# Kernel optimization log

Hardware: AMD Instinct MI355X
Metric: run time of the kernel (lower is better)

## Reference

```python
import jax, jax.numpy as jnp
import numpy as np

D_STATE = 32

def _layernorm(x, g, b, eps=1e-5):
    m = jnp.mean(x, -1, keepdims=True)
    v = jnp.mean((x - m) ** 2, -1, keepdims=True)
    return (x - m) * jax.lax.rsqrt(v + eps) * g + b

def _mlp(x, W1, b1, W2, b2):
    return jax.nn.relu(x @ W1 + b1) @ W2 + b2

def _mamba_block(x, Win, Wconv, bconv, Wxproj, Wdt, bdt, Alog, Dp, Wout):
    Bsz, T, _ = x.shape
    d_inner = Wconv.shape[0]
    dt_rank = Wdt.shape[0]
    xz = x @ Win                                   # [B,T,2*d_inner]
    xi, res = jnp.split(xz, 2, axis=-1)
    K = Wconv.shape[1]
    xp = jnp.pad(xi, ((0, 0), (K - 1, 0), (0, 0)))  # causal depthwise conv
    xi = sum(xp[:, k:k + T, :] * Wconv[:, k] for k in range(K)) + bconv
    xi = jax.nn.silu(xi)
    xdbl = xi @ Wxproj                              # [B,T,dt_rank+2*ds]
    dtr = xdbl[..., :dt_rank]
    Bm = xdbl[..., dt_rank:dt_rank + D_STATE]
    Cm = xdbl[..., dt_rank + D_STATE:]
    dt = jax.nn.softplus(dtr @ Wdt + bdt)           # [B,T,d_inner]
    A = -jnp.exp(Alog)                              # [d_inner, ds]

    def step(h, inp):
        dt_t, B_t, C_t, x_t = inp                   # [B,di],[B,ds],[B,ds],[B,di]
        dA = jnp.exp(dt_t[:, :, None] * A)          # [B,di,ds]
        dBx = (dt_t * x_t)[:, :, None] * B_t[:, None, :]
        h = dA * h + dBx
        return h, jnp.einsum('bds,bs->bd', h, C_t)

    h0 = jnp.zeros((Bsz, d_inner, D_STATE), xi.dtype)
    _, ys = jax.lax.scan(step, h0, (jnp.swapaxes(dt, 0, 1), jnp.swapaxes(Bm, 0, 1),
                                    jnp.swapaxes(Cm, 0, 1), jnp.swapaxes(xi, 0, 1)))
    y = jnp.swapaxes(ys, 0, 1) + xi * Dp
    y = y * jax.nn.silu(res)
    return y @ Wout

def _dynamics(z, Win, Wconv, bconv, Wxproj, Wdt, bdt, Alog, Dp, Wout, gamma, beta):
    out = z
    for i in range(Win.shape[0]):  # 2 stacked residual Mamba blocks
        out = out + _mamba_block(out, Win[i], Wconv[i], bconv[i], Wxproj[i],
                                 Wdt[i], bdt[i], Alog[i], Dp[i], Wout[i])
    return _layernorm(out, gamma, beta)

def setup_inputs():
    key = jax.random.key(0)
    Bz, T, IN, D, DI, DTR, K, NB = 8, 1024, 32, 64, 128, 4, 4, 2
    ks = iter(jax.random.split(key, 32))
    n = lambda shape, s=0.02: jax.random.normal(next(ks), shape, jnp.float32) * s
    return {
        'x': jax.random.normal(next(ks), (Bz, T, IN), jnp.float32),
        'We1': n((IN, 64)), 'be1': jnp.zeros((64,)),
        'We2': n((64, D)), 'be2': jnp.zeros((D,)),
        'Wd1': n((D, 64)), 'bd1': jnp.zeros((64,)),
        'Wd2': n((64, IN)), 'bd2': jnp.zeros((IN,)),
        'Win': n((NB, D, 2 * DI)),
        'Wconv': n((NB, DI, K), 0.1), 'bconv': jnp.zeros((NB, DI)),
        'Wxproj': n((NB, DI, DTR + 2 * D_STATE)),
        'Wdt': n((NB, DTR, DI), 0.1), 'bdt': jnp.full((NB, DI), -4.0),
        'Alog': jnp.tile(jnp.log(jnp.arange(1.0, 33.0)), (NB, DI, 1)),
        'Dparam': jnp.ones((NB, DI)),
        'Wout': n((NB, DI, D)),
        'gamma': jnp.ones((D,)), 'beta': jnp.zeros((D,)),
        'pred_len': 4,
    }

def reference(x, We1, be1, We2, be2, Wd1, bd1, Wd2, bd2, Win, Wconv, bconv,
              Wxproj, Wdt, bdt, Alog, Dparam, Wout, gamma, beta, pred_len):
    z = _mlp(x, We1, be1, We2, be2)
    x_rec = _mlp(z, Wd1, bd1, Wd2, bd2)
    dyn = lambda u: _dynamics(u, Win, Wconv, bconv, Wxproj, Wdt, bdt,
                              Alog, Dparam, Wout, gamma, beta)
    z_dyn = dyn(z)
    x_dyn = _mlp(z_dyn, Wd1, bd1, Wd2, bd2)
    x_pred = None
    if pred_len > 0:
        T = z.shape[1]
        curr = z
        preds = []
        for _ in range(pred_len):
            z_next = dyn(curr[:, -T:, :])[:, -1:, :]
            preds.append(z_next)
            curr = jnp.concatenate([curr, z_next], axis=1)
        x_pred = _mlp(jnp.concatenate(preds, axis=1), Wd1, bd1, Wd2, bd2)
    return (x_rec, x_dyn, x_pred, z, z_dyn)
```

## Files before the change

### kernel.cpp

```cpp
#include <hip/hip_runtime.h>

#define BSZ 8
#define TLEN 1024
#define DM 64
#define DI 128
#define DS 32
#define NCHUNK 16
#define CLEN 64
#define GEXT 1028

__device__ __forceinline__ float siluf(float x) { return x / (1.f + expf(-x)); }
__device__ __forceinline__ float softplusf(float x) { return (x > 20.f) ? x : log1pf(expf(x)); }

__global__ __launch_bounds__(256) void enc_xrec_kernel(
    const float* __restrict__ x,
    const float* __restrict__ We1, const float* __restrict__ be1,
    const float* __restrict__ We2, const float* __restrict__ be2,
    const float* __restrict__ Wd1, const float* __restrict__ bd1,
    const float* __restrict__ Wd2, const float* __restrict__ bd2,
    float* __restrict__ z, float* __restrict__ x_rec)
{
  __shared__ float s_x[16*32];
  __shared__ float s_h1[16*64];
  __shared__ float s_z[16*64];
  __shared__ float s_h2[16*64];
  const int tid = threadIdx.x;
  const int t0 = blockIdx.x * 16;
  s_x[tid]       = x[(size_t)t0*32 + tid];
  s_x[tid + 256] = x[(size_t)t0*32 + tid + 256];
  __syncthreads();
  const int j = tid & 63, tg = tid >> 6;
  {
    float w[32];
    #pragma unroll
    for (int k = 0; k < 32; k++) w[k] = We1[k*64 + j];
    #pragma unroll
    for (int q = 0; q < 4; q++) {
      int t = tg*4 + q;
      float a = be1[j];
      #pragma unroll
      for (int k = 0; k < 32; k++) a = fmaf(s_x[t*32 + k], w[k], a);
      s_h1[t*64 + j] = fmaxf(a, 0.f);
    }
  }
  __syncthreads();
  {
    float w[64];
    #pragma unroll
    for (int k = 0; k < 64; k++) w[k] = We2[k*64 + j];
    #pragma unroll
    for (int q = 0; q < 4; q++) {
      int t = tg*4 + q;
      float a = be2[j];
      #pragma unroll
      for (int k = 0; k < 64; k++) a = fmaf(s_h1[t*64 + k], w[k], a);
      s_z[t*64 + j] = a;
      z[(size_t)(t0 + t)*64 + j] = a;
    }
  }
  __syncthreads();
  {
    float w[64];
    #pragma unroll
    for (int k = 0; k < 64; k++) w[k] = Wd1[k*64 + j];
    #pragma unroll
    for (int q = 0; q < 4; q++) {
      int t = tg*4 + q;
      float a = bd1[j];
      #pragma unroll
      for (int k = 0; k < 64; k++) a = fmaf(s_z[t*64 + k], w[k], a);
      s_h2[t*64 + j] = fmaxf(a, 0.f);
    }
  }
  __syncthreads();
  {
    const int c = tid & 31, tg2 = tid >> 5;
    float w[64];
    #pragma unroll
    for (int k = 0; k < 64; k++) w[k] = Wd2[k*32 + c];
    #pragma unroll
    for (int q = 0; q < 2; q++) {
      int t = tg2*2 + q;
      float a = bd2[c];
      #pragma unroll
      for (int k = 0; k < 64; k++) a = fmaf(s_h2[t*64 + k], w[k], a);
      x_rec[(size_t)(t0 + t)*32 + c] = a;
    }
  }
}

__global__ __launch_bounds__(256,4) void pre_kernel(
    const float* __restrict__ in, int in_stride,
    const float* __restrict__ Win, const float* __restrict__ Wconv, const float* __restrict__ bconv,
    const float* __restrict__ Wxproj, const float* __restrict__ Wdt, const float* __restrict__ bdt,
    float* __restrict__ xibuf, float* __restrict__ resgbuf,
    float2* __restrict__ ddbuf, float* __restrict__ Bbuf, float* __restrict__ Cbuf,
    float* __restrict__ xzout)
{
  __shared__ float s_xi[8*128];
  __shared__ float s_dtr[8*4];
  const int tid = threadIdx.x;
  const int b  = blockIdx.x >> 7;
  const int t0 = (blockIdx.x & 127) * 8;

  const float* rowp[11];
  #pragma unroll
  for (int r = 0; r < 11; r++) {
    int tg = t0 - 3 + r;
    rowp[r] = (tg >= 0) ? in + ((size_t)b*in_stride + tg)*DM : in;
  }

  float acc[11];
  #pragma unroll
  for (int r = 0; r < 11; r++) acc[r] = 0.f;

  if (t0 > 0) {
    #pragma unroll
    for (int k4 = 0; k4 < 16; k4++) {
      float w0 = Win[(k4*4+0)*256 + tid];
      float w1 = Win[(k4*4+1)*256 + tid];
      float w2 = Win[(k4*4+2)*256 + tid];
      float w3 = Win[(k4*4+3)*256 + tid];
      #pragma unroll
      for (int r = 0; r < 11; r++) {
        float4 xv = *(const float4*)(rowp[r] + k4*4);
        acc[r] = fmaf(xv.x, w0, acc[r]);
        acc[r] = fmaf(xv.y, w1, acc[r]);
        acc[r] = fmaf(xv.z, w2, acc[r]);
        acc[r] = fmaf(xv.w, w3, acc[r]);
      }
    }
  } else {
    #pragma unroll
    for (int k4 = 0; k4 < 16; k4++) {
      float w0 = Win[(k4*4+0)*256 + tid];
      float w1 = Win[(k4*4+1)*256 + tid];
      float w2 = Win[(k4*4+2)*256 + tid];
      float w3 = Win[(k4*4+3)*256 + tid];
      #pragma unroll
      for (int r = 3; r < 11; r++) {
        float4 xv = *(const float4*)(rowp[r] + k4*4);
        acc[r] = fmaf(xv.x, w0, acc[r]);
        acc[r] = fmaf(xv.y, w1, acc[r]);
        acc[r] = fmaf(xv.z, w2, acc[r]);
        acc[r] = fmaf(xv.w, w3, acc[r]);
      }
    }
  }

  if (tid < 128) {
    float4 wc = *(const float4*)&Wconv[tid*4];
    float bc = bconv[tid];
    const bool store_xz = (t0 == TLEN-8);
    #pragma unroll
    for (int tau = 0; tau < 8; tau++) {
      float v = bc;
      v = fmaf(acc[tau+0], wc.x, v);
      v = fmaf(acc[tau+1], wc.y, v);
      v = fmaf(acc[tau+2], wc.z, v);
      v = fmaf(acc[tau+3], wc.w, v);
      float xiv = siluf(v);
      s_xi[tau*128 + tid] = xiv;
      xibuf[((size_t)b*TLEN + t0 + tau)*DI + tid] = xiv;
      if (store_xz) xzout[((size_t)b*GEXT + t0 + tau)*128 + tid] = acc[tau+3];
    }
  } else {
    int d = tid - 128;
    #pragma unroll
    for (int tau = 0; tau < 8; tau++)
      resgbuf[((size_t)b*TLEN + t0 + tau)*DI + d] = siluf(acc[tau+3]);
  }
  __syncthreads();
  {
    const int wv = tid >> 6, c = tid & 63;
    float a0 = 0.f, a1 = 0.f;
    const float4* x0 = (const float4*)&s_xi[(wv*2+0)*128];
    const float4* x1 = (const float4*)&s_xi[(wv*2+1)*128];
    #pragma unroll 4
    for (int k4 = 0; k4 < 32; k4++) {
      float wq0 = Wxproj[(k4*4+0)*68 + 4 + c];
      float wq1 = Wxproj[(k4*4+1)*68 + 4 + c];
      float wq2 = Wxproj[(k4*4+2)*68 + 4 + c];
      float wq3 = Wxproj[(k4*4+3)*68 + 4 + c];
      float4 v0 = x0[k4], v1 = x1[k4];
      a0 = fmaf(v0.x,wq0, fmaf(v0.y,wq1, fmaf(v0.z,wq2, fmaf(v0.w,wq3, a0))));
      a1 = fmaf(v1.x,wq0, fmaf(v1.y,wq1, fmaf(v1.z,wq2, fmaf(v1.w,wq3, a1))));
    }
    size_t tb = (size_t)b*TLEN + t0 + wv*2;
    if (c < 32) {
      Bbuf[(tb+0)*DS + c] = a0; Bbuf[(tb+1)*DS + c] = a1;
    } else {
      int cc = c - 32;
      Cbuf[(tb+0)*DS + cc] = a0; Cbuf[(tb+1)*DS + cc] = a1;
    }
  }
  if (tid < 32) {
    int tau = tid >> 2, cc = tid & 3;
    float a = 0.f;
    const float4* xx = (const float4*)&s_xi[tau*128];
    #pragma unroll 4
    for (int k4 = 0; k4 < 32; k4++) {
      float4 v = xx[k4];
      a = fmaf(v.x, Wxproj[(k4*4+0)*68 + cc], a);
      a = fmaf(v.y, Wxproj[(k4*4+1)*68 + cc], a);
      a = fmaf(v.z, Wxproj[(k4*4+2)*68 + cc], a);
      a = fmaf(v.w, Wxproj[(k4*4+3)*68 + cc], a);
    }
    s_dtr[tau*4 + cc] = a;
  }
  __syncthreads();
  #pragma unroll
  for (int u = 0; u < 4; u++) {
    int i = tid + u*256;
    int tau = i >> 7, d = i & 127;
    float a = bdt[d];
    #pragma unroll
    for (int r = 0; r < 4; r++) a = fmaf(s_dtr[tau*4 + r], Wdt[r*128 + d], a);
    float dtv = softplusf(a);
    ddbuf[((size_t)b*TLEN + t0 + tau)*DI + d] = make_float2(dtv, dtv * s_xi[i]);
  }
}

#define BSWZ(row3) (((row3)&3)<<1)

__device__ __forceinline__ int xcd_wid_4096() {
  return (blockIdx.x >> 3) | ((blockIdx.x & 7) << 9);
}

__global__ __launch_bounds__(128) void scan1_kernel(
    const float2* __restrict__ ddbuf, const float* __restrict__ Bbuf,
    const float* __restrict__ Alog, float2* __restrict__ hc)
{
  __shared__ float2 s_dd[4][CLEN];
  __shared__ float  s_Bt[32][68];
  const int tid = threadIdx.x;
  const int ch = tid >> 5, s = tid & 31;
  const int wid = xcd_wid_4096();
  const int dg = wid & 31;
  const int c  = (wid >> 5) & 15;
  const int b  = wid >> 9;
  const int d0 = dg * 4;
  const float A = -__expf(Alog[(d0 + ch)*DS + s]);
  const float2* ddg = ddbuf + ((size_t)b*TLEN + c*CLEN)*DI + d0;
  const float*  Bg  = Bbuf  + ((size_t)b*TLEN + c*CLEN)*DS;
  {
    int t = tid >> 1, half = tid & 1;
    float4 rdd = *(const float4*)((const float*)(ddg + (size_t)t*DI) + half*4);
    s_dd[2*half+0][t] = make_float2(rdd.x, rdd.y);
    s_dd[2*half+1][t] = make_float2(rdd.z, rdd.w);
    #pragma unroll
    for (int j = 0; j < 4; j++) {
      int q = tid + 128*j; int tt = q >> 3, k4 = q & 7;
      float4 rB = *(const float4*)(Bg + tt*DS + k4*4);
      int cp = (((tt>>2) ^ BSWZ(k4>>1)) << 2) + (tt & 3);
      s_Bt[k4*4+0][cp] = rB.x; s_Bt[k4*4+1][cp] = rB.y;
      s_Bt[k4*4+2][cp] = rB.z; s_Bt[k4*4+3][cp] = rB.w;
    }
  }
  __syncthreads();
  float h = 0.f, dts = 0.f;
  const float4* dd4 = (const float4*)&s_dd[ch][0];
  const float4* bt4 = (const float4*)&s_Bt[s][0];
  const int swr = BSWZ(s>>3);
  #pragma unroll
  for (int j = 0; j < 8; j++) {
    float4 e0 = dd4[4*j+0], e1 = dd4[4*j+1], e2 = dd4[4*j+2], e3 = dd4[4*j+3];
    float4 bb0 = bt4[(2*j)^swr], bb1 = bt4[(2*j+1)^swr];
    h = fmaf(__expf(e0.x*A), h, e0.y*bb0.x);
    h = fmaf(__expf(e0.z*A), h, e0.w*bb0.y);
    h = fmaf(__expf(e1.x*A), h, e1.y*bb0.z);
    h = fmaf(__expf(e1.z*A), h, e1.w*bb0.w);
    h = fmaf(__expf(e2.x*A), h, e2.y*bb1.x);
    h = fmaf(__expf(e2.z*A), h, e2.w*bb1.y);
    h = fmaf(__expf(e3.x*A), h, e3.y*bb1.z);
    h = fmaf(__expf(e3.z*A), h, e3.w*bb1.w);
    dts += (e0.x + e0.z) + (e1.x + e1.z) + (e2.x + e2.z) + (e3.x + e3.z);
  }
  int o = ((b*NCHUNK + c)*DI + d0 + ch)*DS + s;
  hc[o] = make_float2(h, __expf(A*dts));
}

__global__ __launch_bounds__(128) void scan3_kernel(
    const float2* __restrict__ ddbuf, const float* __restrict__ Bbuf, const float* __restrict__ Cbuf,
    const float* __restrict__ Alog, const float2* __restrict__ hc, float* __restrict__ ysbuf,
    float* __restrict__ hout)
{
  __shared__ float2 s_dd[4][CLEN];
  __shared__ float  s_Bt[32][68];
  __shared__ float  s_Ct[32][68];
  __shared__ float  s_p[128][33];
  const int tid = threadIdx.x;
  const int ch = tid >> 5, s = tid & 31;
  const int wid = xcd_wid_4096();
  const int dg = wid & 31;
  const int c  = (wid >> 5) & 15;
  const int b  = wid >> 9;
  const int d0 = dg * 4;
  const float A = -__expf(Alog[(d0 + ch)*DS + s]);
  const float2* ddg = ddbuf + ((size_t)b*TLEN + c*CLEN)*DI + d0;
  const float*  Bg  = Bbuf  + ((size_t)b*TLEN + c*CLEN)*DS;
  const float*  Cg  = Cbuf  + ((size_t)b*TLEN + c*CLEN)*DS;

  const int ob = (d0 + ch)*DS + s;
  float2 v[15];
  #pragma unroll
  for (int q = 0; q < 15; q++) v[q] = hc[(size_t)(b*NCHUNK + q)*4096 + ob];

  {
    int t = tid >> 1, half = tid & 1;
    float4 rdd = *(const float4*)((const float*)(ddg + (size_t)t*DI) + half*4);
    s_dd[2*half+0][t] = make_float2(rdd.x, rdd.y);
    s_dd[2*half+1][t] = make_float2(rdd.z, rdd.w);
    #pragma unroll
    for (int j = 0; j < 4; j++) {
      int q = tid + 128*j; int tt = q >> 3, k4 = q & 7;
      float4 rB = *(const float4*)(Bg + tt*DS + k4*4);
      float4 rC = *(const float4*)(Cg + tt*DS + k4*4);
      int cp = (((tt>>2) ^ BSWZ(k4>>1)) << 2) + (tt & 3);
      s_Bt[k4*4+0][cp] = rB.x; s_Bt[k4*4+1][cp] = rB.y;
      s_Bt[k4*4+2][cp] = rB.z; s_Bt[k4*4+3][cp] = rB.w;
      s_Ct[k4*4+0][cp] = rC.x; s_Ct[k4*4+1][cp] = rC.y;
      s_Ct[k4*4+2][cp] = rC.z; s_Ct[k4*4+3][cp] = rC.w;
    }
  }
  float h = 0.f;
  #pragma unroll
  for (int q = 0; q < 15; q++)
    if (q < c) h = fmaf(v[q].y, h, v[q].x);
  __syncthreads();

  const float4* dd4 = (const float4*)&s_dd[ch][0];
  const float4* bt4 = (const float4*)&s_Bt[s][0];
  const float4* ct4 = (const float4*)&s_Ct[s][0];
  const int swr = BSWZ(s>>3);
  float* pr = &s_p[tid][0];
  #pragma unroll
  for (int half = 0; half < 2; half++) {
    #pragma unroll
    for (int j = 0; j < 4; j++) {
      const int jj = half*4 + j;
      float4 e0 = dd4[4*jj+0], e1 = dd4[4*jj+1], e2 = dd4[4*jj+2], e3 = dd4[4*jj+3];
      float4 bb0 = bt4[(2*jj)^swr], bb1 = bt4[(2*jj+1)^swr];
      float4 cc0 = ct4[(2*jj)^swr], cc1 = ct4[(2*jj+1)^swr];
      h = fmaf(__expf(e0.x*A), h, e0.y*bb0.x); pr[8*j+0] = h*cc0.x;
      h = fmaf(__expf(e0.z*A), h, e0.w*bb0.y); pr[8*j+1] = h*cc0.y;
      h = fmaf(__expf(e1.x*A), h, e1.y*bb0.z); pr[8*j+2] = h*cc0.z;
      h = fmaf(__expf(e1.z*A), h, e1.w*bb0.w); pr[8*j+3] = h*cc0.w;
      h = fmaf(__expf(e2.x*A), h, e2.y*bb1.x); pr[8*j+4] = h*cc1.x;
      h = fmaf(__expf(e2.z*A), h, e2.w*bb1.y); pr[8*j+5] = h*cc1.y;
      h = fmaf(__expf(e3.x*A), h, e3.y*bb1.z); pr[8*j+6] = h*cc1.z;
      h = fmaf(__expf(e3.z*A), h, e3.w*bb1.w); pr[8*j+7] = h*cc1.w;
    }
    __syncthreads();
    {
      const int ch2 = tid & 3;
      const int tq  = tid >> 2;
      float a = 0.f;
      #pragma unroll
      for (int s2 = 0; s2 < 32; s2++) a += s_p[ch2*32 + s2][tq];
      ysbuf[(size_t)(b*TLEN + c*CLEN + half*32 + tq)*DI + d0 + ch2] = a;
    }
    __syncthreads();
  }
  if (c == 15) hout[(size_t)(b*DI + d0 + ch)*DS + s] = h;
}

__global__ __launch_bounds__(256,4) void post_kernel(
    const float* __restrict__ ysbuf, const float* __restrict__ xibuf, const float* __restrict__ resgbuf,
    const float* __restrict__ Dp, const float* __restrict__ Wout,
    const float* __restrict__ basebuf, int base_stride,
    float* __restrict__ curg, float* __restrict__ zdyn, float* __restrict__ predz,
    const float* __restrict__ gamma, const float* __restrict__ beta,
    const float* __restrict__ Wd1, const float* __restrict__ bd1,
    const float* __restrict__ Wd2, const float* __restrict__ bd2,
    float* __restrict__ xdyn, int mode)
{
  __shared__ float s_y[8*128];
  __shared__ float s_z[8*64];
  __shared__ float s_h[8*64];
  const int tid = threadIdx.x;
  const int b  = blockIdx.x >> 7;
  const int t0 = (blockIdx.x & 127) * 8;
  #pragma unroll
  for (int u = 0; u < 4; u++) {
    int i = tid + u*256;
    size_t g = (size_t)(b*TLEN + t0)*DI + i;
    s_y[i] = (ysbuf[g] + xibuf[g]*Dp[i & 127]) * resgbuf[g];
  }
  __syncthreads();
  #pragma unroll
  for (int u = 0; u < 2; u++) {
    int i = tid + u*256;
    int tau = i >> 6, c = i & 63;
    float a = 0.f;
    const float4* yy = (const float4*)&s_y[tau*128];
    #pragma unroll 4
    for (int k4 = 0; k4 < 32; k4++) {
      float4 vv = yy[k4];
      a = fmaf(vv.x, Wout[(k4*4+0)*64 + c], a);
      a = fmaf(vv.y, Wout[(k4*4+1)*64 + c], a);
      a = fmaf(vv.z, Wout[(k4*4+2)*64 + c], a);
      a = fmaf(vv.w, Wout[(k4*4+3)*64 + c], a);
    }
    float base = basebuf[((size_t)b*base_stride + t0 + tau)*DM + c];
    float val = base + a;
    if (mode == 0) {
      curg[((size_t)b*GEXT + t0 + tau)*DM + c] = val;
    } else {
      float sum = val;
      #pragma unroll
      for (int m = 1; m < 64; m <<= 1) sum += __shfl_xor(sum, m);
      float mean = sum * (1.f/64.f);
      float dv = val - mean;
      float vs = dv*dv;
      #pragma unroll
      for (int m = 1; m < 64; m <<= 1) vs += __shfl_xor(vs, m);
      float oln = dv * rsqrtf(vs*(1.f/64.f) + 1e-5f) * gamma[c] + beta[c];
      zdyn[(size_t)(b*TLEN + t0 + tau)*DM + c] = oln;
      s_z[tau*64 + c] = oln;
      if (t0 + tau == TLEN-1) predz[(size_t)(b*4 + 0)*DM + c] = oln;
    }
  }
  if (mode == 1) {
    __syncthreads();
    #pragma unroll
    for (int u = 0; u < 2; u++) {
      int i = tid + u*256;
      int t = i >> 6, j = i & 63;
      float a = bd1[j];
      const float4* zz = (const float4*)&s_z[t*64];
      #pragma unroll 4
      for (int k4 = 0; k4 < 16; k4++) {
        float4 zv = zz[k4];
        a = fmaf(zv.x, Wd1[(k4*4+0)*64 + j], a);
        a = fmaf(zv.y, Wd1[(k4*4+1)*64 + j], a);
        a = fmaf(zv.z, Wd1[(k4*4+2)*64 + j], a);
        a = fmaf(zv.w, Wd1[(k4*4+3)*64 + j], a);
      }
      s_h[i] = fmaxf(a, 0.f);
    }
    __syncthreads();
    {
      int t = tid >> 5, c = tid & 31;
      float a = bd2[c];
      const float4* hh = (const float4*)&s_h[t*64];
      #pragma unroll 4
      for (int k4 = 0; k4 < 16; k4++) {
        float4 hv = hh[k4];
        a = fmaf(hv.x, Wd2[(k4*4+0)*32 + c], a);
        a = fmaf(hv.y, Wd2[(k4*4+1)*32 + c], a);
        a = fmaf(hv.z, Wd2[(k4*4+2)*32 + c], a);
        a = fmaf(hv.w, Wd2[(k4*4+3)*32 + c], a);
      }
      xdyn[(size_t)(b*TLEN + t0 + t)*32 + c] = a;
    }
  }
}

__device__ __forceinline__ void mamba_token(
    int tid, int b, int gn, const float* __restrict__ s_in,
    float* __restrict__ xzg, float* __restrict__ hbuf,
    const float* __restrict__ Win, const float* __restrict__ Wcv, const float* __restrict__ bcv,
    const float* __restrict__ Wxp, const float* __restrict__ Wdt, const float* __restrict__ bdt,
    const float* __restrict__ Al, const float* __restrict__ Dpp, const float* __restrict__ Wo,
    float* __restrict__ s_xz, float* __restrict__ s_xi, float* __restrict__ s_rg,
    float* __restrict__ s_dt, float* __restrict__ s_B, float* __restrict__ s_C,
    float* __restrict__ s_dtr, float* __restrict__ s_yp, float* __restrict__ s_y,
    float* __restrict__ s_ssm)
{
  {
    float a = 0.f;
    #pragma unroll
    for (int k = 0; k < 64; k++) a = fmaf(s_in[k], Win[k*256 + tid], a);
    s_xz[tid] = a;
  }
  __syncthreads();
  if (tid < 128) {
    xzg[((size_t)b*GEXT + gn)*128 + tid] = s_xz[tid];
    float acc = bcv[tid];
    acc = fmaf(xzg[((size_t)b*GEXT + gn-3)*128 + tid], Wcv[tid*4+0], acc);
    acc = fmaf(xzg[((size_t)b*GEXT + gn-2)*128 + tid], Wcv[tid*4+1], acc);
    acc = fmaf(xzg[((size_t)b*GEXT + gn-1)*128 + tid], Wcv[tid*4+2], acc);
    acc = fmaf(s_xz[tid], Wcv[tid*4+3], acc);
    s_xi[tid] = siluf(acc);
    s_rg[tid] = siluf(s_xz[128 + tid]);
  }
  __syncthreads();
  if (tid < 68) {
    float a = 0.f;
    #pragma unroll 4
    for (int k = 0; k < 128; k++) a = fmaf(s_xi[k], Wxp[k*68 + tid], a);
    if (tid < 4)       s_dtr[tid] = a;
    else if (tid < 36) s_B[tid-4] = a;
    else               s_C[tid-36] = a;
  }
  __syncthreads();
  if (tid < 128) {
    float a = bdt[tid];
    #pragma unroll
    for (int r = 0; r < 4; r++) a = fmaf(s_dtr[r], Wdt[r*128 + tid], a);
    s_dt[tid] = softplusf(a);
  }
  __syncthreads();
  {
    int d = tid >> 1, sh = (tid & 1) * 16;
    float dtd = s_dt[d], dtxd = dtd * s_xi[d];
    float yp = 0.f;
    #pragma unroll
    for (int q = 0; q < 16; q++) {
      int s = sh + q;
      size_t oo = (size_t)(b*DI + d)*DS + s;
      float A = -__expf(Al[d*DS + s]);
      float h = hbuf[oo];
      h = fmaf(__expf(dtd*A), h, dtxd*s_B[s]);
      hbuf[oo] = h;
      yp = fmaf(s_C[s], h, yp);
    }
    s_yp[(tid & 1)*128 + d] = yp;
  }
  __syncthreads();
  if (tid < 128) s_y[tid] = ((s_yp[tid] + s_yp[128 + tid]) + s_xi[tid]*Dpp[tid]) * s_rg[tid];
  __syncthreads();
  if (tid < 64) {
    float a = 0.f;
    #pragma unroll 4
    for (int k = 0; k < 128; k++) a = fmaf(s_y[k], Wo[k*64 + tid], a);
    s_ssm[tid] = a;
  }
  __syncthreads();
}

__global__ __launch_bounds__(256) void ext_all_kernel(
    float* __restrict__ predz,
    float* __restrict__ xz0, float* __restrict__ xz1,
    float* __restrict__ hbuf0, float* __restrict__ hbuf1,
    const float* __restrict__ Win0, const float* __restrict__ Wcv0, const float* __restrict__ bcv0,
    const float* __restrict__ Wxp0, const float* __restrict__ Wdt0, const float* __restrict__ bdt0,
    const float* __restrict__ Al0, const float* __restrict__ Dp0, const float* __restrict__ Wo0,
    const float* __restrict__ Win1, const float* __restrict__ Wcv1, const float* __restrict__ bcv1,
    const float* __restrict__ Wxp1, const float* __restrict__ Wdt1, const float* __restrict__ bdt1,
    const float* __restrict__ Al1, const float* __restrict__ Dp1, const float* __restrict__ Wo1,
    const float* __restrict__ gamma, const float* __restrict__ beta,
    const float* __restrict__ Wd1, const float* __restrict__ bd1,
    const float* __restrict__ Wd2, const float* __restrict__ bd2,
    float* __restrict__ x_pred)
{
  __shared__ float s_in[64], s_cg[64], s_ssm[64];
  __shared__ float s_xz[256], s_yp[256];
  __shared__ float s_xi[128], s_rg[128], s_dt[128], s_y[128];
  __shared__ float s_B[32], s_C[32], s_dtr[4];
  __shared__ float s_pz[4][64];
  __shared__ float s_h[4][64];
  const int tid = threadIdx.x;
  const int b = blockIdx.x;

  if (tid < 64) s_pz[0][tid] = predz[(size_t)(b*4 + 0)*DM + tid];
  __syncthreads();

  for (int p = 1; p <= 3; p++) {
    const int gn = 1023 + p;
    if (tid < 64) s_in[tid] = s_pz[p-1][tid];
    __syncthreads();
    mamba_token(tid, b, gn, s_in, xz0, hbuf0, Win0, Wcv0, bcv0, Wxp0, Wdt0, bdt0,
                Al0, Dp0, Wo0, s_xz, s_xi, s_rg, s_dt, s_B, s_C, s_dtr, s_yp, s_y, s_ssm);
    if (tid < 64) {
      float cg = s_in[tid] + s_ssm[tid];
      s_cg[tid] = cg;
      s_in[tid] = cg;
    }
    __syncthreads();
    mamba_token(tid, b, gn, s_in, xz1, hbuf1, Win1, Wcv1, bcv1, Wxp1, Wdt1, bdt1,
                Al1, Dp1, Wo1, s_xz, s_xi, s_rg, s_dt, s_B, s_C, s_dtr, s_yp, s_y, s_ssm);
    if (tid < 64) {
      float val = s_cg[tid] + s_ssm[tid];
      float sum = val;
      #pragma unroll
      for (int m = 1; m < 64; m <<= 1) sum += __shfl_xor(sum, m);
      float mean = sum * (1.f/64.f);
      float dv = val - mean;
      float vs = dv*dv;
      #pragma unroll
      for (int m = 1; m < 64; m <<= 1) vs += __shfl_xor(vs, m);
      float oln = dv * rsqrtf(vs*(1.f/64.f) + 1e-5f) * gamma[tid] + beta[tid];
      predz[(size_t)(b*4 + p)*DM + tid] = oln;
      s_pz[p][tid] = oln;
    }
    __syncthreads();
  }

  {
    int t = tid >> 6, j = tid & 63;
    float a = bd1[j];
    const float4* zz = (const float4*)&s_pz[t][0];
    #pragma unroll 4
    for (int k4 = 0; k4 < 16; k4++) {
      float4 zv = zz[k4];
      a = fmaf(zv.x, Wd1[(k4*4+0)*64 + j], a);
      a = fmaf(zv.y, Wd1[(k4*4+1)*64 + j], a);
      a = fmaf(zv.z, Wd1[(k4*4+2)*64 + j], a);
      a = fmaf(zv.w, Wd1[(k4*4+3)*64 + j], a);
    }
    s_h[t][j] = fmaxf(a, 0.f);
  }
  __syncthreads();
  if (tid < 128) {
    int t = tid >> 5, c = tid & 31;
    float a = bd2[c];
    const float4* hh = (const float4*)&s_h[t][0];
    #pragma unroll 4
    for (int k4 = 0; k4 < 16; k4++) {
      float4 hv = hh[k4];
      a = fmaf(hv.x, Wd2[(k4*4+0)*32 + c], a);
      a = fmaf(hv.y, Wd2[(k4*4+1)*32 + c], a);
      a = fmaf(hv.z, Wd2[(k4*4+2)*32 + c], a);
      a = fmaf(hv.w, Wd2[(k4*4+3)*32 + c], a);
    }
    x_pred[(size_t)(b*4 + t)*32 + c] = a;
  }
}

extern "C" void kernel_launch(void* const* d_in, const int* in_sizes, int n_in,
                              void* d_out, int out_size, void* d_ws, size_t ws_size,
                              hipStream_t stream)
{
  (void)in_sizes; (void)n_in; (void)out_size; (void)ws_size;
  const float* x     = (const float*)d_in[0];
  const float* We1   = (const float*)d_in[1];
  const float* be1   = (const float*)d_in[2];
  const float* We2   = (const float*)d_in[3];
  const float* be2   = (const float*)d_in[4];
  const float* Wd1   = (const float*)d_in[5];
  const float* bd1   = (const float*)d_in[6];
  const float* Wd2   = (const float*)d_in[7];
  const float* bd2   = (const float*)d_in[8];
  const float* Win   = (const float*)d_in[9];
  const float* Wconv = (const float*)d_in[10];
  const float* bconv = (const float*)d_in[11];
  const float* Wxp   = (const float*)d_in[12];
  const float* Wdt   = (const float*)d_in[13];
  const float* bdt   = (const float*)d_in[14];
  const float* Alog  = (const float*)d_in[15];
  const float* Dp    = (const float*)d_in[16];
  const float* Wout  = (const float*)d_in[17];
  const float* gamma = (const float*)d_in[18];
  const float* beta  = (const float*)d_in[19];

  float* o      = (float*)d_out;
  float* x_rec  = o;
  float* x_dyn  = o + 262144;
  float* x_pred = o + 524288;
  float* z      = o + 525312;
  float* zdyn   = o + 1049600;

  float* w      = (float*)d_ws;
  float* xi0    = w;
  float* resg0  = xi0   + 1048576;
  float2* dd0   = (float2*)(resg0 + 1048576);
  float* Bb0    = resg0 + 1048576 + 2097152;
  float* Cb0    = Bb0   + 262144;
  float* xi1    = Cb0   + 262144;
  float* resg1  = xi1   + 1048576;
  float2* dd1   = (float2*)(resg1 + 1048576);
  float* Bb1    = resg1 + 1048576 + 2097152;
  float* Cb1    = Bb1   + 262144;
  float* ys     = Cb1   + 262144;
  float2* hc    = (float2*)(ys + 1048576);
  float* predz  = ys + 1048576 + 1048576;
  float* xz0    = predz + 2048;
  float* xz1    = xz0   + 1052672;
  float* curg   = xz1   + 1052672;
  float* hbuf0  = curg  + 526336;
  float* hbuf1  = hbuf0 + 32768;

  const float* Win0 = Win,   *Win1 = Win + 64*256;
  const float* Wcv0 = Wconv, *Wcv1 = Wconv + 128*4;
  const float* bcv0 = bconv, *bcv1 = bconv + 128;
  const float* Wxp0 = Wxp,   *Wxp1 = Wxp + 128*68;
  const float* Wdt0 = Wdt,   *Wdt1 = Wdt + 4*128;
  const float* bdt0 = bdt,   *bdt1 = bdt + 128;
  const float* Al0  = Alog,  *Al1  = Alog + 128*32;
  const float* Dp0  = Dp,    *Dp1  = Dp + 128;
  const float* Wo0  = Wout,  *Wo1  = Wout + 128*64;

  enc_xrec_kernel<<<dim3(512), dim3(256), 0, stream>>>(x, We1, be1, We2, be2, Wd1, bd1, Wd2, bd2, z, x_rec);

  pre_kernel<<<dim3(1024), dim3(256), 0, stream>>>(z, TLEN,
                                                   Win0, Wcv0, bcv0, Wxp0, Wdt0, bdt0,
                                                   xi0, resg0, dd0, Bb0, Cb0, xz0);
  scan1_kernel<<<dim3(4096), dim3(128), 0, stream>>>(dd0, Bb0, Al0, hc);
  scan3_kernel<<<dim3(4096), dim3(128), 0, stream>>>(dd0, Bb0, Cb0, Al0, hc, ys, hbuf0);
  post_kernel<<<dim3(1024), dim3(256), 0, stream>>>(ys, xi0, resg0, Dp0, Wo0,
                                                    z, TLEN, curg,
                                                    (float*)nullptr, (float*)nullptr,
                                                    (const float*)nullptr, (const float*)nullptr,
                                                    (const float*)nullptr, (const float*)nullptr,
                                                    (const float*)nullptr, (const float*)nullptr,
                                                    (float*)nullptr, 0);

  pre_kernel<<<dim3(1024), dim3(256), 0, stream>>>(curg, GEXT,
                                                   Win1, Wcv1, bcv1, Wxp1, Wdt1, bdt1,
                                                   xi1, resg1, dd1, Bb1, Cb1, xz1);
  scan1_kernel<<<dim3(4096), dim3(128), 0, stream>>>(dd1, Bb1, Al1, hc);
  scan3_kernel<<<dim3(4096), dim3(128), 0, stream>>>(dd1, Bb1, Cb1, Al1, hc, ys, hbuf1);
  post_kernel<<<dim3(1024), dim3(256), 0, stream>>>(ys, xi1, resg1, Dp1, Wo1,
                                                    curg, GEXT, (float*)nullptr,
                                                    zdyn, predz, gamma, beta,
                                                    Wd1, bd1, Wd2, bd2, x_dyn, 1);

  ext_all_kernel<<<dim3(8), dim3(256), 0, stream>>>(predz, xz0, xz1, hbuf0, hbuf1,
      Win0, Wcv0, bcv0, Wxp0, Wdt0, bdt0, Al0, Dp0, Wo0,
      Win1, Wcv1, bcv1, Wxp1, Wdt1, bdt1, Al1, Dp1, Wo1,
      gamma, beta, Wd1, bd1, Wd2, bd2, x_pred);
}
```

Measured before the change: 235.1 us.

## Fuse encoder MLP into block-0 pre kernel and block-0 post into block-1 pre

Merges the encoder/reconstruction MLP kernel with the first Mamba pre-processing kernel, and the first block's output projection/residual with the second block's pre-processing. Each fused block recomputes the 3 halo rows needed by the causal conv in shared memory instead of re-reading z/curg from global memory. This removes two kernel launches and the global round trips of z and curg as inputs, at the cost of redundant halo computation (11 rows for 8 tokens) and more shared memory per block.

After: 228.6 us. -2.7%, faster.

```diff
diff --git a/kernel.cpp b/kernel.cpp
--- a/kernel.cpp
+++ b/kernel.cpp
@@ -12,139 +12,31 @@
 __device__ __forceinline__ float siluf(float x) { return x / (1.f + expf(-x)); }
 __device__ __forceinline__ float softplusf(float x) { return (x > 20.f) ? x : log1pf(expf(x)); }
 
-__global__ __launch_bounds__(256) void enc_xrec_kernel(
-    const float* __restrict__ x,
-    const float* __restrict__ We1, const float* __restrict__ be1,
-    const float* __restrict__ We2, const float* __restrict__ be2,
-    const float* __restrict__ Wd1, const float* __restrict__ bd1,
-    const float* __restrict__ Wd2, const float* __restrict__ bd2,
-    float* __restrict__ z, float* __restrict__ x_rec)
-{
-  __shared__ float s_x[16*32];
-  __shared__ float s_h1[16*64];
-  __shared__ float s_z[16*64];
-  __shared__ float s_h2[16*64];
-  const int tid = threadIdx.x;
-  const int t0 = blockIdx.x * 16;
-  s_x[tid]       = x[(size_t)t0*32 + tid];
-  s_x[tid + 256] = x[(size_t)t0*32 + tid + 256];
-  __syncthreads();
-  const int j = tid & 63, tg = tid >> 6;
-  {
-    float w[32];
-    #pragma unroll
-    for (int k = 0; k < 32; k++) w[k] = We1[k*64 + j];
-    #pragma unroll
-    for (int q = 0; q < 4; q++) {
-      int t = tg*4 + q;
-      float a = be1[j];
-      #pragma unroll
-      for (int k = 0; k < 32; k++) a = fmaf(s_x[t*32 + k], w[k], a);
-      s_h1[t*64 + j] = fmaxf(a, 0.f);
-    }
-  }
-  __syncthreads();
-  {
-    float w[64];
-    #pragma unroll
-    for (int k = 0; k < 64; k++) w[k] = We2[k*64 + j];
-    #pragma unroll
-    for (int q = 0; q < 4; q++) {
-      int t = tg*4 + q;
-      float a = be2[j];
-      #pragma unroll
-      for (int k = 0; k < 64; k++) a = fmaf(s_h1[t*64 + k], w[k], a);
-      s_z[t*64 + j] = a;
-      z[(size_t)(t0 + t)*64 + j] = a;
-    }
-  }
-  __syncthreads();
-  {
-    float w[64];
-    #pragma unroll
-    for (int k = 0; k < 64; k++) w[k] = Wd1[k*64 + j];
-    #pragma unroll
-    for (int q = 0; q < 4; q++) {
-      int t = tg*4 + q;
-      float a = bd1[j];
-      #pragma unroll
-      for (int k = 0; k < 64; k++) a = fmaf(s_z[t*64 + k], w[k], a);
-      s_h2[t*64 + j] = fmaxf(a, 0.f);
-    }
-  }
-  __syncthreads();
-  {
-    const int c = tid & 31, tg2 = tid >> 5;
-    float w[64];
-    #pragma unroll
-    for (int k = 0; k < 64; k++) w[k] = Wd2[k*32 + c];
-    #pragma unroll
-    for (int q = 0; q < 2; q++) {
-      int t = tg2*2 + q;
-      float a = bd2[c];
-      #pragma unroll
-      for (int k = 0; k < 64; k++) a = fmaf(s_h2[t*64 + k], w[k], a);
-      x_rec[(size_t)(t0 + t)*32 + c] = a;
-    }
-  }
-}
-
-__global__ __launch_bounds__(256,4) void pre_kernel(
-    const float* __restrict__ in, int in_stride,
+__device__ __forceinline__ void pre_tail(
+    int tid, int b, int t0, const float* __restrict__ s_zrows,
+    float* __restrict__ s_xi, float* __restrict__ s_dtr,
     const float* __restrict__ Win, const float* __restrict__ Wconv, const float* __restrict__ bconv,
     const float* __restrict__ Wxproj, const float* __restrict__ Wdt, const float* __restrict__ bdt,
     float* __restrict__ xibuf, float* __restrict__ resgbuf,
     float2* __restrict__ ddbuf, float* __restrict__ Bbuf, float* __restrict__ Cbuf,
     float* __restrict__ xzout)
 {
-  __shared__ float s_xi[8*128];
-  __shared__ float s_dtr[8*4];
-  const int tid = threadIdx.x;
-  const int b  = blockIdx.x >> 7;
-  const int t0 = (blockIdx.x & 127) * 8;
-
-  const float* rowp[11];
-  #pragma unroll
-  for (int r = 0; r < 11; r++) {
-    int tg = t0 - 3 + r;
-    rowp[r] = (tg >= 0) ? in + ((size_t)b*in_stride + tg)*DM : in;
-  }
-
   float acc[11];
   #pragma unroll
   for (int r = 0; r < 11; r++) acc[r] = 0.f;
-
-  if (t0 > 0) {
-    #pragma unroll
-    for (int k4 = 0; k4 < 16; k4++) {
-      float w0 = Win[(k4*4+0)*256 + tid];
-      float w1 = Win[(k4*4+1)*256 + tid];
-      float w2 = Win[(k4*4+2)*256 + tid];
-      float w3 = Win[(k4*4+3)*256 + tid];
-      #pragma unroll
-      for (int r = 0; r < 11; r++) {
-        float4 xv = *(const float4*)(rowp[r] + k4*4);
-        acc[r] = fmaf(xv.x, w0, acc[r]);
-        acc[r] = fmaf(xv.y, w1, acc[r]);
-        acc[r] = fmaf(xv.z, w2, acc[r]);
-        acc[r] = fmaf(xv.w, w3, acc[r]);
-      }
-    }
-  } else {
-    #pragma unroll
-    for (int k4 = 0; k4 < 16; k4++) {
-      float w0 = Win[(k4*4+0)*256 + tid];
-      float w1 = Win[(k4*4+1)*256 + tid];
-      float w2 = Win[(k4*4+2)*256 + tid];
-      float w3 = Win[(k4*4+3)*256 + tid];
-      #pragma unroll
-      for (int r = 3; r < 11; r++) {
-        float4 xv = *(const float4*)(rowp[r] + k4*4);
-        acc[r] = fmaf(xv.x, w0, acc[r]);
-        acc[r] = fmaf(xv.y, w1, acc[r]);
-        acc[r] = fmaf(xv.z, w2, acc[r]);
-        acc[r] = fmaf(xv.w, w3, acc[r]);
-      }
+  #pragma unroll
+  for (int k4 = 0; k4 < 16; k4++) {
+    float w0 = Win[(k4*4+0)*256 + tid];
+    float w1 = Win[(k4*4+1)*256 + tid];
+    float w2 = Win[(k4*4+2)*256 + tid];
+    float w3 = Win[(k4*4+3)*256 + tid];
+    #pragma unroll
+    for (int r = 0; r < 11; r++) {
+      float4 xv = *(const float4*)&s_zrows[r*64 + k4*4];
+      acc[r] = fmaf(xv.x, w0, acc[r]);
+      acc[r] = fmaf(xv.y, w1, acc[r]);
+      acc[r] = fmaf(xv.z, w2, acc[r]);
+      acc[r] = fmaf(xv.w, w3, acc[r]);
     }
   }
 
@@ -219,6 +111,183 @@
     float dtv = softplusf(a);
     ddbuf[((size_t)b*TLEN + t0 + tau)*DI + d] = make_float2(dtv, dtv * s_xi[i]);
   }
+}
+
+__global__ __launch_bounds__(256,4) void encpre_kernel(
+    const float* __restrict__ x,
+    const float* __restrict__ We1, const float* __restrict__ be1,
+    const float* __restrict__ We2, const float* __restrict__ be2,
+    const float* __restrict__ Wd1, const float* __restrict__ bd1,
+    const float* __restrict__ Wd2, const float* __restrict__ bd2,
+    float* __restrict__ zout, float* __restrict__ x_rec,
+    const float* __restrict__ Win, const float* __restrict__ Wconv, const float* __restrict__ bconv,
+    const float* __restrict__ Wxproj, const float* __restrict__ Wdt, const float* __restrict__ bdt,
+    float* __restrict__ xibuf, float* __restrict__ resgbuf,
+    float2* __restrict__ ddbuf, float* __restrict__ Bbuf, float* __restrict__ Cbuf,
+    float* __restrict__ xzout)
+{
+  __shared__ float s_x[11*32];
+  __shared__ float s_h1[11*64];
+  __shared__ float s_z[11*64];
+  __shared__ float s_h2[8*64];
+  __shared__ float s_xi[8*128];
+  __shared__ float s_dtr[8*4];
+  const int tid = threadIdx.x;
+  const int b  = blockIdx.x >> 7;
+  const int t0 = (blockIdx.x & 127) * 8;
+
+  for (int i = tid; i < 11*32; i += 256) {
+    int r = i >> 5, c = i & 31;
+    int tg = t0 - 3 + r;
+    s_x[i] = (tg >= 0) ? x[(size_t)(b*TLEN + tg)*32 + c] : 0.f;
+  }
+  __syncthreads();
+  {
+    const int j = tid & 63, tg4 = tid >> 6;
+    #pragma unroll
+    for (int q = 0; q < 3; q++) {
+      int r = tg4 + 4*q;
+      if (r < 11) {
+        float a = be1[j];
+        const float4* xx = (const float4*)&s_x[r*32];
+        #pragma unroll
+        for (int k4 = 0; k4 < 8; k4++) {
+          float4 v = xx[k4];
+          a = fmaf(v.x, We1[(k4*4+0)*64 + j], a);
+          a = fmaf(v.y, We1[(k4*4+1)*64 + j], a);
+          a = fmaf(v.z, We1[(k4*4+2)*64 + j], a);
+          a = fmaf(v.w, We1[(k4*4+3)*64 + j], a);
+        }
+        s_h1[r*64 + j] = fmaxf(a, 0.f);
+      }
+    }
+  }
+  __syncthreads();
+  {
+    const int j = tid & 63, tg4 = tid >> 6;
+    #pragma unroll
+    for (int q = 0; q < 3; q++) {
+      int r = tg4 + 4*q;
+      if (r < 11) {
+        float a;
+        if (t0 == 0 && r < 3) {
+          a = 0.f;
+        } else {
+          a = be2[j];
+          const float4* hh = (const float4*)&s_h1[r*64];
+          #pragma unroll 4
+          for (int k4 = 0; k4 < 16; k4++) {
+            float4 v = hh[k4];
+            a = fmaf(v.x, We2[(k4*4+0)*64 + j], a);
+            a = fmaf(v.y, We2[(k4*4+1)*64 + j], a);
+            a = fmaf(v.z, We2[(k4*4+2)*64 + j], a);
+            a = fmaf(v.w, We2[(k4*4+3)*64 + j], a);
+          }
+        }
+        s_z[r*64 + j] = a;
+        if (r >= 3) zout[(size_t)(b*TLEN + t0 + r-3)*64 + j] = a;
+      }
+    }
+  }
+  __syncthreads();
+  {
+    const int j = tid & 63, tg4 = tid >> 6;
+    #pragma unroll
+    for (int q = 0; q < 2; q++) {
+      int t = tg4 + 4*q;
+      float a = bd1[j];
+      const float4* zz = (const float4*)&s_z[(t+3)*64];
+      #pragma unroll 4
+      for (int k4 = 0; k4 < 16; k4++) {
+        float4 v = zz[k4];
+        a = fmaf(v.x, Wd1[(k4*4+0)*64 + j], a);
+        a = fmaf(v.y, Wd1[(k4*4+1)*64 + j], a);
+        a = fmaf(v.z, Wd1[(k4*4+2)*64 + j], a);
+        a = fmaf(v.w, Wd1[(k4*4+3)*64 + j], a);
+      }
+      s_h2[t*64 + j] = fmaxf(a, 0.f);
+    }
+  }
+  __syncthreads();
+  {
+    int t = tid >> 5, c = tid & 31;
+    float a = bd2[c];
+    const float4* hh = (const float4*)&s_h2[t*64];
+    #pragma unroll 4
+    for (int k4 = 0; k4 < 16; k4++) {
+      float4 v = hh[k4];
+      a = fmaf(v.x, Wd2[(k4*4+0)*32 + c], a);
+      a = fmaf(v.y, Wd2[(k4*4+1)*32 + c], a);
+      a = fmaf(v.z, Wd2[(k4*4+2)*32 + c], a);
+      a = fmaf(v.w, Wd2[(k4*4+3)*32 + c], a);
+    }
+    x_rec[(size_t)(b*TLEN + t0 + t)*32 + c] = a;
+  }
+  pre_tail(tid, b, t0, s_z, s_xi, s_dtr,
+           Win, Wconv, bconv, Wxproj, Wdt, bdt,
+           xibuf, resgbuf, ddbuf, Bbuf, Cbuf, xzout);
+}
+
+__global__ __launch_bounds__(256,4) void postpre_kernel(
+    const float* __restrict__ ys, const float* __restrict__ xi0, const float* __restrict__ resg0,
+    const float* __restrict__ Dp0, const float* __restrict__ Wo0,
+    const float* __restrict__ zsrc,
+    const float* __restrict__ Win, const float* __restrict__ Wconv, const float* __restrict__ bconv,
+    const float* __restrict__ Wxproj, const float* __restrict__ Wdt, const float* __restrict__ bdt,
+    float* __restrict__ curg,
+    float* __restrict__ xibuf, float* __restrict__ resgbuf,
+    float2* __restrict__ ddbuf, float* __restrict__ Bbuf, float* __restrict__ Cbuf,
+    float* __restrict__ xzout)
+{
+  __shared__ float s_y[11*128];
+  __shared__ float s_cur[11*64];
+  __shared__ float s_xi[8*128];
+  __shared__ float s_dtr[8*4];
+  const int tid = threadIdx.x;
+  const int b  = blockIdx.x >> 7;
+  const int t0 = (blockIdx.x & 127) * 8;
+
+  for (int i = tid; i < 11*128; i += 256) {
+    int r = i >> 7, d = i & 127;
+    int tg = t0 - 3 + r;
+    float v = 0.f;
+    if (tg >= 0) {
+      size_t g = (size_t)(b*TLEN + tg)*DI + d;
+      v = (ys[g] + xi0[g]*Dp0[d]) * resg0[g];
+    }
+    s_y[i] = v;
+  }
+  __syncthreads();
+  {
+    const int c = tid & 63, tg4 = tid >> 6;
+    #pragma unroll
+    for (int q = 0; q < 3; q++) {
+      int r = tg4 + 4*q;
+      if (r < 11) {
+        int tg = t0 - 3 + r;
+        float val = 0.f;
+        if (tg >= 0) {
+          float a = 0.f;
+          const float4* yy = (const float4*)&s_y[r*128];
+          #pragma unroll 4
+          for (int k4 = 0; k4 < 32; k4++) {
+            float4 vv = yy[k4];
+            a = fmaf(vv.x, Wo0[(k4*4+0)*64 + c], a);
+            a = fmaf(vv.y, Wo0[(k4*4+1)*64 + c], a);
+            a = fmaf(vv.z, Wo0[(k4*4+2)*64 + c], a);
+            a = fmaf(vv.w, Wo0[(k4*4+3)*64 + c], a);
+          }
+          val = zsrc[(size_t)(b*TLEN + tg)*DM + c] + a;
+          if (r >= 3) curg[((size_t)b*GEXT + tg)*DM + c] = val;
+        }
+        s_cur[r*64 + c] = val;
+      }
+    }
+  }
+  __syncthreads();
+  pre_tail(tid, b, t0, s_cur, s_xi, s_dtr,
+           Win, Wconv, bconv, Wxproj, Wdt, bdt,
+           xibuf, resgbuf, ddbuf, Bbuf, Cbuf, xzout);
 }
 
 #define BSWZ(row3) (((row3)&3)<<1)
@@ -369,11 +438,11 @@
     const float* __restrict__ ysbuf, const float* __restrict__ xibuf, const float* __restrict__ resgbuf,
     const float* __restrict__ Dp, const float* __restrict__ Wout,
     const float* __restrict__ basebuf, int base_stride,
-    float* __restrict__ curg, float* __restrict__ zdyn, float* __restrict__ predz,
+    float* __restrict__ zdyn, float* __restrict__ predz,
     const float* __restrict__ gamma, const float* __restrict__ beta,
     const float* __restrict__ Wd1, const float* __restrict__ bd1,
     const float* __restrict__ Wd2, const float* __restrict__ bd2,
-    float* __restrict__ xdyn, int mode)
+    float* __restrict__ xdyn)
 {
   __shared__ float s_y[8*128];
   __shared__ float s_z[8*64];
@@ -404,56 +473,50 @@
     }
     float base = basebuf[((size_t)b*base_stride + t0 + tau)*DM + c];
     float val = base + a;
-    if (mode == 0) {
-      curg[((size_t)b*GEXT + t0 + tau)*DM + c] = val;
-    } else {
-      float sum = val;
-      #pragma unroll
-      for (int m = 1; m < 64; m <<= 1) sum += __shfl_xor(sum, m);
-      float mean = sum * (1.f/64.f);
-      float dv = val - mean;
-      float vs = dv*dv;
-      #pragma unroll
-      for (int m = 1; m < 64; m <<= 1) vs += __shfl_xor(vs, m);
-      float oln = dv * rsqrtf(vs*(1.f/64.f) + 1e-5f) * gamma[c] + beta[c];
-      zdyn[(size_t)(b*TLEN + t0 + tau)*DM + c] = oln;
-      s_z[tau*64 + c] = oln;
-      if (t0 + tau == TLEN-1) predz[(size_t)(b*4 + 0)*DM + c] = oln;
-    }
-  }
-  if (mode == 1) {
-    __syncthreads();
-    #pragma unroll
-    for (int u = 0; u < 2; u++) {
-      int i = tid + u*256;
-      int t = i >> 6, j = i & 63;
-      float a = bd1[j];
-      const float4* zz = (const float4*)&s_z[t*64];
-      #pragma unroll 4
-      for (int k4 = 0; k4 < 16; k4++) {
-        float4 zv = zz[k4];
-        a = fmaf(zv.x, Wd1[(k4*4+0)*64 + j], a);
-        a = fmaf(zv.y, Wd1[(k4*4+1)*64 + j], a);
-        a = fmaf(zv.z, Wd1[(k4*4+2)*64 + j], a);
-        a = fmaf(zv.w, Wd1[(k4*4+3)*64 + j], a);
-      }
-      s_h[i] = fmaxf(a, 0.f);
-    }
-    __syncthreads();
-    {
-      int t = tid >> 5, c = tid & 31;
-      float a = bd2[c];
-      const float4* hh = (const float4*)&s_h[t*64];
-      #pragma unroll 4
-      for (int k4 = 0; k4 < 16; k4++) {
-        float4 hv = hh[k4];
-        a = fmaf(hv.x, Wd2[(k4*4+0)*32 + c], a);
-        a = fmaf(hv.y, Wd2[(k4*4+1)*32 + c], a);
-        a = fmaf(hv.z, Wd2[(k4*4+2)*32 + c], a);
-        a = fmaf(hv.w, Wd2[(k4*4+3)*32 + c], a);
-      }
-      xdyn[(size_t)(b*TLEN + t0 + t)*32 + c] = a;
-    }
+    float sum = val;
+    #pragma unroll
+    for (int m = 1; m < 64; m <<= 1) sum += __shfl_xor(sum, m);
+    float mean = sum * (1.f/64.f);
+    float dv = val - mean;
+    float vs = dv*dv;
+    #pragma unroll
+    for (int m = 1; m < 64; m <<= 1) vs += __shfl_xor(vs, m);
+    float oln = dv * rsqrtf(vs*(1.f/64.f) + 1e-5f) * gamma[c] + beta[c];
+    zdyn[(size_t)(b*TLEN + t0 + tau)*DM + c] = oln;
+    s_z[tau*64 + c] = oln;
+    if (t0 + tau == TLEN-1) predz[(size_t)(b*4 + 0)*DM + c] = oln;
+  }
+  __syncthreads();
+  #pragma unroll
+  for (int u = 0; u < 2; u++) {
+    int i = tid + u*256;
+    int t = i >> 6, j = i & 63;
+    float a = bd1[j];
+    const float4* zz = (const float4*)&s_z[t*64];
+    #pragma unroll 4
+    for (int k4 = 0; k4 < 16; k4++) {
+      float4 zv = zz[k4];
+      a = fmaf(zv.x, Wd1[(k4*4+0)*64 + j], a);
+      a = fmaf(zv.y, Wd1[(k4*4+1)*64 + j], a);
+      a = fmaf(zv.z, Wd1[(k4*4+2)*64 + j], a);
+      a = fmaf(zv.w, Wd1[(k4*4+3)*64 + j], a);
+    }
+    s_h[i] = fmaxf(a, 0.f);
+  }
+  __syncthreads();
+  {
+    int t = tid >> 5, c = tid & 31;
+    float a = bd2[c];
+    const float4* hh = (const float4*)&s_h[t*64];
+    #pragma unroll 4
+    for (int k4 = 0; k4 < 16; k4++) {
+      float4 hv = hh[k4];
+      a = fmaf(hv.x, Wd2[(k4*4+0)*32 + c], a);
+      a = fmaf(hv.y, Wd2[(k4*4+1)*32 + c], a);
+      a = fmaf(hv.z, Wd2[(k4*4+2)*32 + c], a);
+      a = fmaf(hv.w, Wd2[(k4*4+3)*32 + c], a);
+    }
+    xdyn[(size_t)(b*TLEN + t0 + t)*32 + c] = a;
   }
 }
 
@@ -682,30 +745,24 @@
   const float* Dp0  = Dp,    *Dp1  = Dp + 128;
   const float* Wo0  = Wout,  *Wo1  = Wout + 128*64;
 
-  enc_xrec_kernel<<<dim3(512), dim3(256), 0, stream>>>(x, We1, be1, We2, be2, Wd1, bd1, Wd2, bd2, z, x_rec);
-
-  pre_kernel<<<dim3(1024), dim3(256), 0, stream>>>(z, TLEN,
-                                                   Win0, Wcv0, bcv0, Wxp0, Wdt0, bdt0,
-                                                   xi0, resg0, dd0, Bb0, Cb0, xz0);
+  encpre_kernel<<<dim3(1024), dim3(256), 0, stream>>>(x, We1, be1, We2, be2, Wd1, bd1, Wd2, bd2,
+                                                      z, x_rec,
+                                                      Win0, Wcv0, bcv0, Wxp0, Wdt0, bdt0,
+                                                      xi0, resg0, dd0, Bb0, Cb0, xz0);
   scan1_kernel<<<dim3(4096), dim3(128), 0, stream>>>(dd0, Bb0, Al0, hc);
   scan3_kernel<<<dim3(4096), dim3(128), 0, stream>>>(dd0, Bb0, Cb0, Al0, hc, ys, hbuf0);
-  post_kernel<<<dim3(1024), dim3(256), 0, stream>>>(ys, xi0, resg0, Dp0, Wo0,
-                                                    z, TLEN, curg,
-                                                    (float*)nullptr, (float*)nullptr,
-                                                    (const float*)nullptr, (const float*)nullptr,
-                                                    (const float*)nullptr, (const float*)nullptr,
-                                                    (const float*)nullptr, (const float*)nullptr,
-                                                    (float*)nullptr, 0);
-
-  pre_kernel<<<dim3(1024), dim3(256), 0, stream>>>(curg, GEXT,
-                                                   Win1, Wcv1, bcv1, Wxp1, Wdt1, bdt1,
-                                                   xi1, resg1, dd1, Bb1, Cb1, xz1);
+
+  postpre_kernel<<<dim3(1024), dim3(256), 0, stream>>>(ys, xi0, resg0, Dp0, Wo0, z,
+                                                       Win1, Wcv1, bcv1, Wxp1, Wdt1, bdt1,
+                                                       curg,
+                                                       xi1, resg1, dd1, Bb1, Cb1, xz1);
   scan1_kernel<<<dim3(4096), dim3(128), 0, stream>>>(dd1, Bb1, Al1, hc);
   scan3_kernel<<<dim3(4096), dim3(128), 0, stream>>>(dd1, Bb1, Cb1, Al1, hc, ys, hbuf1);
+
   post_kernel<<<dim3(1024), dim3(256), 0, stream>>>(ys, xi1, resg1, Dp1, Wo1,
-                                                    curg, GEXT, (float*)nullptr,
+                                                    curg, GEXT,
                                                     zdyn, predz, gamma, beta,
-                                                    Wd1, bd1, Wd2, bd2, x_dyn, 1);
+                                                    Wd1, bd1, Wd2, bd2, x_dyn);
 
   ext_all_kernel<<<dim3(8), dim3(256), 0, stream>>>(predz, xz0, xz1, hbuf0, hbuf1,
       Win0, Wcv0, bcv0, Wxp0, Wdt0, bdt0, Al0, Dp0, Wo0,
```
